# Kernel tuning notes

Hardware: AMD Instinct MI355X
Metric: run time of the kernel (lower is better)

The kernel has to match this reference:

```python
import jax, jax.numpy as jnp
import numpy as np

B, K, L, D, H = 128, 51, 60, 1, 32
NB = 2  # MAF blocks
LOG2PI = float(np.log(2.0 * np.pi))


def setup_inputs():
    kit = iter(jax.random.split(jax.random.key(0), 64))
    def nrm(shape, s=0.05):
        return jax.random.normal(next(kit), shape, dtype=jnp.float32) * s
    def uni(shape, lo, hi):
        return jax.random.uniform(next(kit), shape, dtype=jnp.float32, minval=lo, maxval=hi)
    c = L * D          # attention feature dim = 60
    KL = K * L         # 3060
    KL32 = KL * 32     # 97920
    return dict(
        x=jax.random.normal(next(kit), (B, K, L, D), dtype=jnp.float32),
        attn_Wq=nrm((c, c), 0.1), attn_bq=nrm((c,), 0.1),
        attn_Wk=nrm((c, c), 0.1), attn_bk=nrm((c,), 0.1),
        lstm_Wih=nrm((4 * H, D), 0.2), lstm_Whh=nrm((4 * H, H), 0.1),
        lstm_bih=nrm((4 * H,), 0.1), lstm_bhh=nrm((4 * H,), 0.1),
        gnn_Wn=nrm((H, H), 0.1), gnn_bn=nrm((H,), 0.1),
        gnn_Wr=nrm((H, H), 0.1),
        gnn_W2=nrm((H, H), 0.1), gnn_b2=nrm((H,), 0.1),
        mlp_W1=nrm((KL, 500), 0.02), mlp_b1=nrm((500,), 0.05),
        bn1_g=uni((500,), 0.8, 1.2), bn1_b=nrm((500,), 0.05),
        bn1_m=nrm((500,), 0.05), bn1_v=uni((500,), 0.5, 1.5),
        mlp_W2=nrm((500, 500), 0.05), mlp_b2=nrm((500,), 0.05),
        bn2_g=uni((500,), 0.8, 1.2), bn2_b=nrm((500,), 0.05),
        bn2_m=nrm((500,), 0.05), bn2_v=uni((500,), 0.5, 1.5),
        mlp_W3=nrm((500, KL32), 0.05), mlp_b3=nrm((KL32,), 0.05),
        ann_W=nrm((KL32, 100), 0.005), ann_b=nrm((100,), 0.05),
        annbn_g=uni((100,), 0.8, 1.2), annbn_b=nrm((100,), 0.05),
        annbn_m=nrm((100,), 0.05), annbn_v=uni((100,), 0.5, 1.5),
        maf_in_W=nrm((NB, H, D), 0.1), maf_in_b=nrm((NB, H), 0.1),
        maf_cond_W=nrm((NB, H, H), 0.1),
        maf_out_W=nrm((NB, 2 * D, H), 0.1), maf_out_b=nrm((NB, 2 * D), 0.1),
        maf_bn_lg=nrm((NB, D), 0.05), maf_bn_beta=nrm((NB, D), 0.05),
    )


def _forward(x, attn_Wq, attn_bq, attn_Wk, attn_bk,
             lstm_Wih, lstm_Whh, lstm_bih, lstm_bhh,
             gnn_Wn, gnn_bn, gnn_Wr, gnn_W2, gnn_b2,
             mlp_W1, mlp_b1, bn1_g, bn1_b, bn1_m, bn1_v,
             mlp_W2, mlp_b2, bn2_g, bn2_b, bn2_m, bn2_v,
             mlp_W3, mlp_b3,
             ann_W, ann_b, annbn_g, annbn_b, annbn_m, annbn_v,
             maf_in_W, maf_in_b, maf_cond_W, maf_out_W, maf_out_b,
             maf_bn_lg, maf_bn_beta):
    Bb, Kk, Ll, Dd = x.shape
    c = Ll * Dd
    # --- ScaleDotProductAttention (eval: dropout = identity) ---
    xf = x.reshape(Bb, Kk, c)
    q = xf @ attn_Wq + attn_bq
    k = xf @ attn_Wk + attn_bk
    k_t = k.reshape(Bb, c, Kk)                 # torch .view -- a reshape, NOT a transpose
    score = (q @ k_t) / jnp.sqrt(jnp.asarray(c, x.dtype))
    graph = jax.nn.softmax(score, axis=1)      # softmax over dim=1, (B,K,K)
    # --- single-layer LSTM over (B*K, L, D) ---
    xs = x.reshape(Bb * Kk, Ll, Dd)
    Hh = lstm_Whh.shape[1]
    def step(carry, xt):
        h, cc = carry
        z = xt @ lstm_Wih.T + lstm_bih + h @ lstm_Whh.T + lstm_bhh
        i, f, g, o = jnp.split(z, 4, axis=-1)  # torch gate order i,f,g,o
        cc = jax.nn.sigmoid(f) * cc + jax.nn.sigmoid(i) * jnp.tanh(g)
        h = jax.nn.sigmoid(o) * jnp.tanh(cc)
        return (h, cc), h
    h0 = jnp.zeros((Bb * Kk, Hh), dtype=x.dtype)
    _, hs = jax.lax.scan(step, (h0, h0), jnp.swapaxes(xs, 0, 1))
    h = jnp.swapaxes(hs, 0, 1).reshape(Bb, Kk, Ll, Hh)  # (B,K,L,H)
    # --- GNN message passing on attention-derived adjacency ---
    agg = jnp.einsum('bkld,bkj->bjld', h, graph)
    h_n = agg @ gnn_Wn + gnn_bn
    h_n = h_n.at[:, :, 1:].add(h[:, :, :-1] @ gnn_Wr)   # temporal shift residual
    h_gcn = jax.nn.relu(h_n) @ gnn_W2 + gnn_b2
    # --- gcn_mlp residual (BatchNorm1d in eval mode) ---
    bn = lambda z, g, b, m, v: (z - m) / jnp.sqrt(v + 1e-5) * g + b
    xflat = xs.reshape(Bb, -1)                          # (B, K*L*D)
    z = bn(jax.nn.relu(xflat @ mlp_W1 + mlp_b1), bn1_g, bn1_b, bn1_m, bn1_v)
    z = bn(jax.nn.relu(z @ mlp_W2 + mlp_b2), bn2_g, bn2_b, bn2_m, bn2_v)
    z = z @ mlp_W3 + mlp_b3
    h_gcn = z.reshape(h_gcn.shape) + h_gcn
    # --- ann head ---
    hid = bn(jax.nn.relu(h_gcn.reshape(Bb, -1) @ ann_W + ann_b),
             annbn_g, annbn_b, annbn_m, annbn_v)
    # --- conditional MAF log-prob over rows of (B*K*L, 1) with cond (., H) ---
    # input_size==1 => MADE output mask is all-zero (output degree -1 < hidden degree 0)
    u = xs.reshape(-1, Dd)
    cond = h_gcn.reshape(-1, h_gcn.shape[-1])
    mask_out = jnp.zeros((2 * Dd, Hh), dtype=x.dtype)
    sum_ldj = jnp.zeros_like(u)
    eps = 1e-5
    for i in range(maf_in_W.shape[0]):
        hm = jnp.tanh(u @ maf_in_W[i].T + maf_in_b[i] + cond @ maf_cond_W[i].T)
        out = hm @ (maf_out_W[i] * mask_out).T + maf_out_b[i]
        m, loga = out[:, :Dd], out[:, Dd:]
        u = (u - m) * jnp.exp(-loga)
        sum_ldj = sum_ldj - loga
        # flow BatchNorm, eval mode (running_mean=0, running_var=1 buffers)
        u = jnp.exp(maf_bn_lg[i]) * u * jax.lax.rsqrt(jnp.asarray(1.0 + eps, x.dtype)) + maf_bn_beta[i]
        sum_ldj = sum_ldj + maf_bn_lg[i] - 0.5 * jnp.log(jnp.asarray(1.0 + eps, x.dtype))
    logp_row = jnp.sum(-0.5 * LOG2PI - 0.5 * u * u + sum_ldj, axis=1)  # (B*K*L,)
    log_prob = logp_row.reshape(Bb, -1).mean(axis=1)    # (B,)
    return hid, log_prob, h_gcn


def reference(x, attn_Wq, attn_bq, attn_Wk, attn_bk,
              lstm_Wih, lstm_Whh, lstm_bih, lstm_bhh,
              gnn_Wn, gnn_bn, gnn_Wr, gnn_W2, gnn_b2,
              mlp_W1, mlp_b1, bn1_g, bn1_b, bn1_m, bn1_v,
              mlp_W2, mlp_b2, bn2_g, bn2_b, bn2_m, bn2_v,
              mlp_W3, mlp_b3,
              ann_W, ann_b, annbn_g, annbn_b, annbn_m, annbn_v,
              maf_in_W, maf_in_b, maf_cond_W, maf_out_W, maf_out_b,
              maf_bn_lg, maf_bn_beta):
    hid, log_prob, h_gcn = _forward(
        x, attn_Wq, attn_bq, attn_Wk, attn_bk,
        lstm_Wih, lstm_Whh, lstm_bih, lstm_bhh,
        gnn_Wn, gnn_bn, gnn_Wr, gnn_W2, gnn_b2,
        mlp_W1, mlp_b1, bn1_g, bn1_b, bn1_m, bn1_v,
        mlp_W2, mlp_b2, bn2_g, bn2_b, bn2_m, bn2_v,
        mlp_W3, mlp_b3,
        ann_W, ann_b, annbn_g, annbn_b, annbn_m, annbn_v,
        maf_in_W, maf_in_b, maf_cond_W, maf_out_W, maf_out_b,
        maf_bn_lg, maf_bn_beta)
    return (hid, log_prob.mean(), h_gcn, log_prob)
```

## Files before the change

kernel.cpp:

```cpp
#include <hip/hip_runtime.h>
#include <math.h>

constexpr int cB = 128;
constexpr int cK = 51;
constexpr int cL = 60;
constexpr int cH = 32;
constexpr int cC = 60;
constexpr int cKL = 3060;
constexpr int cKL32 = 97920;
constexpr float kLOG2PI = 1.8378770664093453f;

typedef __attribute__((ext_vector_type(8))) short bfrag8;
typedef __attribute__((ext_vector_type(16))) float accf16;
typedef __attribute__((ext_vector_type(4))) float accf4;
typedef __attribute__((ext_vector_type(4))) unsigned uint4v;

__device__ __forceinline__ float frcp(float x) { return __builtin_amdgcn_rcpf(x); }
__device__ __forceinline__ float fsig(float x) { return frcp(1.0f + __expf(-x)); }
__device__ __forceinline__ float ftanh(float x) {
  float e = __expf(2.0f * x);
  return 1.0f - 2.0f * frcp(e + 1.0f);
}
__device__ __forceinline__ short f2bf(float f) {
  union { float f; unsigned u; } v; v.f = f;
  unsigned r = v.u + 0x7FFFu + ((v.u >> 16) & 1u);
  return (short)(r >> 16);
}
__device__ __forceinline__ unsigned pk2bf(float lo, float hi) {
  unsigned r;
  asm("v_cvt_pk_bf16_f32 %0, %1, %2" : "=v"(r) : "v"(lo), "v"(hi));
  return r;
}

__global__ __launch_bounds__(256) void qk_kernel(
    const float* __restrict__ x, const float* __restrict__ Wq, const float* __restrict__ bq,
    const float* __restrict__ Wk, const float* __restrict__ bk,
    float* __restrict__ q, float* __restrict__ kx) {
  __shared__ float xs[8][cC];
  const int row0 = blockIdx.x * 8;
  const int tid = threadIdx.x;
  for (int idx = tid; idx < 8 * cC; idx += 256) {
    int lr = idx / cC, t = idx % cC;
    xs[lr][t] = x[(row0 + lr) * cC + t];
  }
  __syncthreads();
  for (int idx = tid; idx < 8 * 2 * cC; idx += 256) {
    int col = idx % cC;
    int r2 = idx / cC;
    int m = r2 & 1, lr = r2 >> 1;
    const float* W = m ? Wk : Wq;
    float acc = m ? bk[col] : bq[col];
    #pragma unroll 4
    for (int t = 0; t < cC; ++t) acc += xs[lr][t] * W[t * cC + col];
    float* outp = m ? kx : q;
    outp[(row0 + lr) * cC + col] = acc;
  }
}

__global__ __launch_bounds__(256) void attn_kernel(
    const float* __restrict__ q, const float* __restrict__ kx, float* __restrict__ graph) {
  __shared__ float qb[cKL];
  __shared__ float kb[cKL];
  __shared__ float sc[cK * cK];
  __shared__ float cmax[cK], csum[cK];
  const int b = blockIdx.x;
  const int tid = threadIdx.x;
  for (int idx = tid; idx < cKL; idx += 256) {
    qb[idx] = q[b * cKL + idx];
    kb[idx] = kx[b * cKL + idx];
  }
  __syncthreads();
  const float scale = 1.0f / sqrtf(60.0f);
  for (int idx = tid; idx < cK * cK; idx += 256) {
    int i = idx / cK, j = idx % cK;
    float acc = 0.0f;
    #pragma unroll 4
    for (int t = 0; t < cC; ++t) acc += qb[i * cC + t] * kb[t * cK + j];
    sc[idx] = acc * scale;
  }
  __syncthreads();
  if (tid < cK) {
    float m = -1e30f;
    for (int i = 0; i < cK; ++i) m = fmaxf(m, sc[i * cK + tid]);
    float ssum = 0.0f;
    for (int i = 0; i < cK; ++i) ssum += __expf(sc[i * cK + tid] - m);
    cmax[tid] = m; csum[tid] = ssum;
  }
  __syncthreads();
  for (int idx = tid; idx < cK * cK; idx += 256) {
    int j = idx % cK;
    graph[b * cK * cK + idx] = __expf(sc[idx] - cmax[j]) / csum[j];
  }
}

__global__ __launch_bounds__(64) void lstm_mfma_kernel(
    const float* __restrict__ x, const float* __restrict__ Wih, const float* __restrict__ Whh,
    const float* __restrict__ bih, const float* __restrict__ bhh, float* __restrict__ hout) {
  __shared__ float xlds[cL][16];
  __shared__ __align__(16) float hlds[16][36];
  const int lane = threadIdx.x;
  const int n = lane & 15;
  const int grp = lane >> 4;
  const int seq0 = blockIdx.x * 16;

  for (int i = lane; i < 16 * cL; i += 64) {
    const int s = i / cL, t = i % cL;
    xlds[t][s] = x[(size_t)(seq0 + s) * cL + t];
  }
  for (int i = lane; i < 16 * 36; i += 64) (&hlds[0][0])[i] = 0.0f;

  bfrag8 bf[8];
  float bias8[8], wih8[8];
  #pragma unroll
  for (int g = 0; g < 8; ++g) {
    const float* wrow = Whh + (g * 16 + n) * cH + grp * 8;
    const float4 p0 = *reinterpret_cast<const float4*>(wrow);
    const float4 p1 = *reinterpret_cast<const float4*>(wrow + 4);
    union { unsigned u[4]; bfrag8 b; } ub;
    ub.u[0] = pk2bf(p0.x, p0.y); ub.u[1] = pk2bf(p0.z, p0.w);
    ub.u[2] = pk2bf(p1.x, p1.y); ub.u[3] = pk2bf(p1.z, p1.w);
    bf[g] = ub.b;
    bias8[g] = bih[g * 16 + n] + bhh[g * 16 + n];
    wih8[g] = Wih[g * 16 + n];
  }
  float cst[8];
  #pragma unroll
  for (int i = 0; i < 8; ++i) cst[i] = 0.0f;
  __syncthreads();

  float* outp = hout + (size_t)seq0 * cL * cH;
  for (int t = 0; t < cL; ++t) {
    const float4 h0 = *reinterpret_cast<const float4*>(&hlds[n][grp * 8]);
    const float4 h1 = *reinterpret_cast<const float4*>(&hlds[n][grp * 8 + 4]);
    union { unsigned u[4]; bfrag8 b; } ua;
    ua.u[0] = pk2bf(h0.x, h0.y); ua.u[1] = pk2bf(h0.z, h0.w);
    ua.u[2] = pk2bf(h1.x, h1.y); ua.u[3] = pk2bf(h1.z, h1.w);
    const float4 xt = *reinterpret_cast<const float4*>(&xlds[t][grp * 4]);
    accf4 acc[8];
    #pragma unroll
    for (int g = 0; g < 8; ++g) {
      accf4 ci;
      ci[0] = fmaf(wih8[g], xt.x, bias8[g]);
      ci[1] = fmaf(wih8[g], xt.y, bias8[g]);
      ci[2] = fmaf(wih8[g], xt.z, bias8[g]);
      ci[3] = fmaf(wih8[g], xt.w, bias8[g]);
      acc[g] = __builtin_amdgcn_mfma_f32_16x16x32_bf16(ua.b, bf[g], ci, 0, 0, 0);
    }
    __builtin_amdgcn_sched_barrier(0);
    #pragma unroll
    for (int hh = 0; hh < 2; ++hh) {
      #pragma unroll
      for (int r = 0; r < 4; ++r) {
        const float iv = acc[0 + hh][r];
        const float fv = acc[2 + hh][r];
        const float gv = acc[4 + hh][r];
        const float ov = acc[6 + hh][r];
        float cs = cst[hh * 4 + r];
        cs = fmaf(fsig(fv), cs, fsig(iv) * ftanh(gv));
        const float hv = fsig(ov) * ftanh(cs);
        cst[hh * 4 + r] = cs;
        hlds[grp * 4 + r][n + hh * 16] = hv;
        outp[(size_t)(grp * 4 + r) * (cL * cH) + t * cH + n + hh * 16] = hv;
      }
    }
    __builtin_amdgcn_sched_barrier(0);
  }
}

__global__ __launch_bounds__(256) void agg_kernel(
    const float* __restrict__ hbuf, const float* __restrict__ graph,
    float* __restrict__ aggout) {
  __shared__ float G[cK * cK];
  __shared__ __align__(16) float Ht[cK][128];
  const int b = blockIdx.y;
  const int c0 = blockIdx.x * 128;
  const int tid = threadIdx.x;
  for (int idx = tid; idx < cK * cK; idx += 256) G[idx] = graph[b * cK * cK + idx];
  for (int idx = tid; idx < cK * 128; idx += 256) {
    int k = idx >> 7, c = idx & 127;
    Ht[k][c] = hbuf[((size_t)b * cK + k) * 1920 + c0 + c];
  }
  __syncthreads();
  const int jg = tid >> 5;
  const int cg = tid & 31;
  const int cc = cg * 4;
  float4 acc[7];
  #pragma unroll
  for (int jj = 0; jj < 7; ++jj) acc[jj] = make_float4(0.f, 0.f, 0.f, 0.f);
  for (int k = 0; k < cK; ++k) {
    const float4 hv = *reinterpret_cast<const float4*>(&Ht[k][cc]);
    #pragma unroll
    for (int jj = 0; jj < 7; ++jj) {
      const int j = jg + jj * 8;
      const float g = (j < cK) ? G[k * cK + j] : 0.0f;
      acc[jj].x += g * hv.x; acc[jj].y += g * hv.y;
      acc[jj].z += g * hv.z; acc[jj].w += g * hv.w;
    }
  }
  #pragma unroll
  for (int jj = 0; jj < 7; ++jj) {
    const int j = jg + jj * 8;
    if (j < cK) {
      const size_t o = ((size_t)b * cK + j) * 1920 + c0 + cc;
      aggout[o + 0] = acc[jj].x; aggout[o + 1] = acc[jj].y;
      aggout[o + 2] = acc[jj].z; aggout[o + 3] = acc[jj].w;
    }
  }
}

__global__ __launch_bounds__(256) void gnn2_kernel(
    const float* __restrict__ hbuf, const float* __restrict__ Wn,
    const float* __restrict__ bn_, const float* __restrict__ Wr,
    const float* __restrict__ W2, const float* __restrict__ b2,
    float* __restrict__ hg) {
  __shared__ __align__(16) float wn[cH * cH];
  __shared__ __align__(16) float wr[cH * cH];
  __shared__ __align__(16) float w2[cH * cH];
  __shared__ float bnb[cH], b2b[cH];
  __shared__ float A_[192][33];
  __shared__ float M_[192][33];
  const int tid = threadIdx.x;
  const int row0 = blockIdx.x * 192;
  for (int idx = tid; idx < cH * cH; idx += 256) { wn[idx] = Wn[idx]; wr[idx] = Wr[idx]; w2[idx] = W2[idx]; }
  if (tid < cH) { bnb[tid] = bn_[tid]; b2b[tid] = b2[tid]; }
  for (int idx = tid; idx < 192 * 32; idx += 256) {
    const int r = idx >> 5, d = idx & 31;
    A_[r][d] = hg[(size_t)(row0 + r) * 32 + d];
    const int g = row0 + r;
    const int l = g % 60;
    M_[r][d] = (l > 0) ? hbuf[(size_t)(g - 1) * 32 + d] : 0.0f;
  }
  __syncthreads();
  const int rg = tid >> 2;
  const int cg = tid & 3;
  const int c0 = cg * 8;
  const int r0 = rg * 3;
  float acc[3][8];
  #pragma unroll
  for (int i = 0; i < 3; ++i)
    #pragma unroll
    for (int d = 0; d < 8; ++d) acc[i][d] = bnb[c0 + d];
  for (int e = 0; e < cH; ++e) {
    const float4 wn0 = *reinterpret_cast<const float4*>(&wn[e * cH + c0]);
    const float4 wn1 = *reinterpret_cast<const float4*>(&wn[e * cH + c0 + 4]);
    const float4 wr0 = *reinterpret_cast<const float4*>(&wr[e * cH + c0]);
    const float4 wr1 = *reinterpret_cast<const float4*>(&wr[e * cH + c0 + 4]);
    #pragma unroll
    for (int i = 0; i < 3; ++i) {
      const float a = A_[r0 + i][e];
      const float m = M_[r0 + i][e];
      acc[i][0] += a * wn0.x + m * wr0.x; acc[i][1] += a * wn0.y + m * wr0.y;
      acc[i][2] += a * wn0.z + m * wr0.z; acc[i][3] += a * wn0.w + m * wr0.w;
      acc[i][4] += a * wn1.x + m * wr1.x; acc[i][5] += a * wn1.y + m * wr1.y;
      acc[i][6] += a * wn1.z + m * wr1.z; acc[i][7] += a * wn1.w + m * wr1.w;
    }
  }
  __syncthreads();
  #pragma unroll
  for (int i = 0; i < 3; ++i)
    #pragma unroll
    for (int d = 0; d < 8; ++d) A_[r0 + i][c0 + d] = fmaxf(acc[i][d], 0.0f);
  __syncthreads();
  float acc2[3][8];
  #pragma unroll
  for (int i = 0; i < 3; ++i)
    #pragma unroll
    for (int d = 0; d < 8; ++d) acc2[i][d] = b2b[c0 + d];
  for (int e = 0; e < cH; ++e) {
    const float4 w20 = *reinterpret_cast<const float4*>(&w2[e * cH + c0]);
    const float4 w21 = *reinterpret_cast<const float4*>(&w2[e * cH + c0 + 4]);
    #pragma unroll
    for (int i = 0; i < 3; ++i) {
      const float t = A_[r0 + i][e];
      acc2[i][0] += t * w20.x; acc2[i][1] += t * w20.y;
      acc2[i][2] += t * w20.z; acc2[i][3] += t * w20.w;
      acc2[i][4] += t * w21.x; acc2[i][5] += t * w21.y;
      acc2[i][6] += t * w21.z; acc2[i][7] += t * w21.w;
    }
  }
  #pragma unroll
  for (int i = 0; i < 3; ++i)
    #pragma unroll
    for (int d = 0; d < 8; ++d) M_[r0 + i][c0 + d] = acc2[i][d];
  __syncthreads();
  for (int idx = tid; idx < 192 * 32; idx += 256) {
    const int r = idx >> 5, d = idx & 31;
    hg[(size_t)row0 * 32 + idx] = M_[r][d];
  }
}

__global__ __launch_bounds__(256) void gemm_splitk_kernel(
    const float* __restrict__ A, const float* __restrict__ W,
    int K, int N, float* __restrict__ partial) {
  __shared__ __align__(16) float At[128][65];
  __shared__ __align__(16) float Wt[64][64];
  const int tid = threadIdx.x;
  const int n0 = blockIdx.x * 64;
  const int k0 = blockIdx.y * 64;
  const int kw = min(64, K - k0);
  for (int idx = tid; idx < 128 * 64; idx += 256) {
    int r = idx >> 6, kk = idx & 63;
    At[r][kk] = (kk < kw) ? A[(size_t)r * K + k0 + kk] : 0.0f;
  }
  for (int idx = tid; idx < 64 * 64; idx += 256) {
    int kk = idx >> 6, cc = idx & 63;
    Wt[kk][cc] = (kk < kw && n0 + cc < N) ? W[(size_t)(k0 + kk) * N + n0 + cc] : 0.0f;
  }
  __syncthreads();
  const int cg = tid & 15, rg = tid >> 4;
  const int c0 = cg * 4, r0 = rg * 8;
  float acc[8][4];
  #pragma unroll
  for (int i = 0; i < 8; ++i)
    #pragma unroll
    for (int jj = 0; jj < 4; ++jj) acc[i][jj] = 0.0f;
  for (int kk = 0; kk < 64; kk += 2) {
    const float4 wv0 = *reinterpret_cast<const float4*>(&Wt[kk][c0]);
    const float4 wv1 = *reinterpret_cast<const float4*>(&Wt[kk + 1][c0]);
    #pragma unroll
    for (int i = 0; i < 8; ++i) {
      const float2 av = *reinterpret_cast<const float2*>(&At[r0 + i][kk]);
      acc[i][0] += av.x * wv0.x + av.y * wv1.x;
      acc[i][1] += av.x * wv0.y + av.y * wv1.y;
      acc[i][2] += av.x * wv0.z + av.y * wv1.z;
      acc[i][3] += av.x * wv0.w + av.y * wv1.w;
    }
  }
  float* p = partial + (size_t)blockIdx.y * 128 * N;
  #pragma unroll
  for (int i = 0; i < 8; ++i) {
    #pragma unroll
    for (int jj = 0; jj < 4; ++jj) {
      const int cc = n0 + c0 + jj;
      if (cc < N) p[(r0 + i) * N + cc] = acc[i][jj];
    }
  }
}

__global__ __launch_bounds__(256) void mlpred_kernel(
    const float* __restrict__ partial, int S, int N,
    const float* __restrict__ bias, const float* __restrict__ gg,
    const float* __restrict__ bb, const float* __restrict__ mm,
    const float* __restrict__ vv, float* __restrict__ outz) {
  const int oi = blockIdx.x * 256 + threadIdx.x;
  if (oi >= 128 * N) return;
  float s = 0.0f;
  for (int p = 0; p < S; ++p) s += partial[(size_t)p * 128 * N + oi];
  const int c = oi % N;
  const float z = fmaxf(s + bias[c], 0.0f);
  outz[oi] = (z - mm[c]) * rsqrtf(vv[c] + 1e-5f) * gg[c] + bb[c];
}

__global__ __launch_bounds__(256) void mlpredbf_kernel(
    const float* __restrict__ partial, int S,
    const float* __restrict__ bias, const float* __restrict__ gg,
    const float* __restrict__ bb, const float* __restrict__ mm,
    const float* __restrict__ vv, unsigned short* __restrict__ outbf) {
  const int oi = blockIdx.x * 256 + threadIdx.x;
  if (oi >= 128 * 512) return;
  const int r = oi >> 9, c = oi & 511;
  unsigned short val = 0;
  if (c < 500) {
    float s = 0.0f;
    for (int p = 0; p < S; ++p) s += partial[(size_t)p * 64000 + r * 500 + c];
    const float z = fmaxf(s + bias[c], 0.0f);
    const float y = (z - mm[c]) * rsqrtf(vv[c] + 1e-5f) * gg[c] + bb[c];
    val = (unsigned short)f2bf(y);
  }
  outbf[oi] = val;
}

__global__ __launch_bounds__(256, 3) void w3_mfma_kernel(
    const unsigned short* __restrict__ z2bf, const float* __restrict__ W3,
    const float* __restrict__ b3, float* __restrict__ outh) {
  __shared__ unsigned Bs[2][16][128];
  const int tid = threadIdx.x;
  const int n0 = blockIdx.x * 128;
  const int wv = tid >> 6;
  const int lane = tid & 63;
  const int half = lane >> 5;
  const int lm = lane & 31;
  const int kp = tid >> 4;
  const int nc = (tid & 15) << 3;

  accf16 acc[4] = {};

  const unsigned short* Ab = z2bf + lm * 512 + half * 8;
  const float* Wp = W3 + (size_t)(2 * kp) * cKL32 + n0 + nc;

  {
    const float4 r0a = *reinterpret_cast<const float4*>(Wp);
    const float4 r0b = *reinterpret_cast<const float4*>(Wp + 4);
    const float4 r1a = *reinterpret_cast<const float4*>(Wp + cKL32);
    const float4 r1b = *reinterpret_cast<const float4*>(Wp + cKL32 + 4);
    uint4v w0 = {pk2bf(r0a.x, r1a.x), pk2bf(r0a.y, r1a.y), pk2bf(r0a.z, r1a.z), pk2bf(r0a.w, r1a.w)};
    uint4v w1 = {pk2bf(r0b.x, r1b.x), pk2bf(r0b.y, r1b.y), pk2bf(r0b.z, r1b.z), pk2bf(r0b.w, r1b.w)};
    *reinterpret_cast<uint4v*>(&Bs[0][kp][nc]) = w0;
    *reinterpret_cast<uint4v*>(&Bs[0][kp][nc + 4]) = w1;
  }
  __syncthreads();

  int cur = 0;
  for (int t = 0; t < 16; ++t) {
    const int k0 = t << 5;
    bfrag8 a0[4], a1[4];
    #pragma unroll
    for (int mf = 0; mf < 4; ++mf) {
      a0[mf] = *reinterpret_cast<const bfrag8*>(Ab + mf * 16384 + k0);
      a1[mf] = *reinterpret_cast<const bfrag8*>(Ab + mf * 16384 + k0 + 16);
    }
    float4 r0a = make_float4(0.f, 0.f, 0.f, 0.f), r0b = r0a, r1a = r0a, r1b = r0a;
    if (t < 15) {
      const int kA = k0 + 32 + 2 * kp;
      const float* p = Wp + (size_t)(k0 + 32) * cKL32;
      if (kA < 500)     { r0a = *reinterpret_cast<const float4*>(p);
                          r0b = *reinterpret_cast<const float4*>(p + 4); }
      if (kA + 1 < 500) { r1a = *reinterpret_cast<const float4*>(p + cKL32);
                          r1b = *reinterpret_cast<const float4*>(p + cKL32 + 4); }
    }
    const unsigned* Bf = &Bs[cur][0][0];
    const int colL = wv * 32 + lm;
    union { unsigned u[4]; bfrag8 b; } cv0, cv1;
    #pragma unroll
    for (int c = 0; c < 4; ++c) cv0.u[c] = Bf[(half * 4 + c) * 128 + colL];
    #pragma unroll
    for (int c = 0; c < 4; ++c) cv1.u[c] = Bf[(8 + half * 4 + c) * 128 + colL];
    #pragma unroll
    for (int mf = 0; mf < 4; ++mf)
      acc[mf] = __builtin_amdgcn_mfma_f32_32x32x16_bf16(a0[mf], cv0.b, acc[mf], 0, 0, 0);
    #pragma unroll
    for (int mf = 0; mf < 4; ++mf)
      acc[mf] = __builtin_amdgcn_mfma_f32_32x32x16_bf16(a1[mf], cv1.b, acc[mf], 0, 0, 0);
    if (t < 15) {
      uint4v w0 = {pk2bf(r0a.x, r1a.x), pk2bf(r0a.y, r1a.y), pk2bf(r0a.z, r1a.z), pk2bf(r0a.w, r1a.w)};
      uint4v w1 = {pk2bf(r0b.x, r1b.x), pk2bf(r0b.y, r1b.y), pk2bf(r0b.z, r1b.z), pk2bf(r0b.w, r1b.w)};
      *reinterpret_cast<uint4v*>(&Bs[cur ^ 1][kp][nc]) = w0;
      *reinterpret_cast<uint4v*>(&Bs[cur ^ 1][kp][nc + 4]) = w1;
    }
    __syncthreads();
    cur ^= 1;
  }

  const int col = n0 + wv * 32 + lm;
  const float bias = b3[col];
  #pragma unroll
  for (int mf = 0; mf < 4; ++mf) {
    #pragma unroll
    for (int reg = 0; reg < 16; ++reg) {
      const int rr = mf * 32 + (reg & 3) + 8 * (reg >> 2) + 4 * half;
      const size_t o = (size_t)rr * cKL32 + col;
      outh[o] += acc[mf][reg] + bias;
    }
  }
}

__global__ __launch_bounds__(256, 3) void ann_mfma_kernel(
    const float* __restrict__ hg, const float* __restrict__ annW,
    float* __restrict__ partial) {
  __shared__ unsigned Bs[2][16][128];
  const int tid = threadIdx.x;
  const int bx = blockIdx.x;
  const int kbase = bx * 128;
  const int wv = tid >> 6;
  const int lane = tid & 63;
  const int half = lane >> 5;
  const int lm = lane & 31;

  accf16 acc[4] = {};

  #pragma unroll
  for (int i = 0; i < 8; ++i) {
    const int idx = tid + i * 256;
    const int kp = idx >> 7, col = idx & 127;
    float w0 = 0.f, w1 = 0.f;
    if (col < 100) {
      const size_t base = (size_t)(kbase + 2 * kp) * 100 + col;
      w0 = annW[base];
      w1 = annW[base + 100];
    }
    Bs[0][kp][col] = pk2bf(w0, w1);
  }
  __syncthreads();

  const float* Ap = hg + (size_t)lm * cKL32 + kbase + half * 8;
  int cur = 0;
  for (int t = 0; t < 4; ++t) {
    const int k0 = t * 32;
    bfrag8 a0[4], a1[4];
    #pragma unroll
    for (int mf = 0; mf < 4; ++mf) {
      const float* p = Ap + (size_t)mf * 32 * cKL32 + k0;
      const float4 f0 = *reinterpret_cast<const float4*>(p);
      const float4 f1 = *reinterpret_cast<const float4*>(p + 4);
      const float4 g0 = *reinterpret_cast<const float4*>(p + 16);
      const float4 g1 = *reinterpret_cast<const float4*>(p + 20);
      union { unsigned u[4]; bfrag8 b; } ua, ub;
      ua.u[0] = pk2bf(f0.x, f0.y); ua.u[1] = pk2bf(f0.z, f0.w);
      ua.u[2] = pk2bf(f1.x, f1.y); ua.u[3] = pk2bf(f1.z, f1.w);
      ub.u[0] = pk2bf(g0.x, g0.y); ub.u[1] = pk2bf(g0.z, g0.w);
      ub.u[2] = pk2bf(g1.x, g1.y); ub.u[3] = pk2bf(g1.z, g1.w);
      a0[mf] = ua.b; a1[mf] = ub.b;
    }
    float w0r[8], w1r[8];
    if (t < 3) {
      #pragma unroll
      for (int i = 0; i < 8; ++i) {
        const int idx = tid + i * 256;
        const int kp = idx >> 7, col = idx & 127;
        w0r[i] = 0.f; w1r[i] = 0.f;
        if (col < 100) {
          const size_t base = (size_t)(kbase + (t + 1) * 32 + 2 * kp) * 100 + col;
          w0r[i] = annW[base];
          w1r[i] = annW[base + 100];
        }
      }
    }
    const unsigned* Bf = &Bs[cur][0][0];
    const int colL = wv * 32 + lm;
    union { unsigned u[4]; bfrag8 b; } cv0, cv1;
    #pragma unroll
    for (int c = 0; c < 4; ++c) cv0.u[c] = Bf[(half * 4 + c) * 128 + colL];
    #pragma unroll
    for (int c = 0; c < 4; ++c) cv1.u[c] = Bf[(8 + half * 4 + c) * 128 + colL];
    #pragma unroll
    for (int mf = 0; mf < 4; ++mf)
      acc[mf] = __builtin_amdgcn_mfma_f32_32x32x16_bf16(a0[mf], cv0.b, acc[mf], 0, 0, 0);
    #pragma unroll
    for (int mf = 0; mf < 4; ++mf)
      acc[mf] = __builtin_amdgcn_mfma_f32_32x32x16_bf16(a1[mf], cv1.b, acc[mf], 0, 0, 0);
    if (t < 3) {
      #pragma unroll
      for (int i = 0; i < 8; ++i) {
        const int idx = tid + i * 256;
        const int kp = idx >> 7, col = idx & 127;
        Bs[cur ^ 1][kp][col] = pk2bf(w0r[i], w1r[i]);
      }
    }
    __syncthreads();
    cur ^= 1;
  }

  const int col = wv * 32 + lm;
  if (col < 100) {
    float* p = partial + (size_t)bx * 12800;
    #pragma unroll
    for (int mf = 0; mf < 4; ++mf) {
      #pragma unroll
      for (int reg = 0; reg < 16; ++reg) {
        const int rr = mf * 32 + (reg & 3) + 8 * (reg >> 2) + 4 * half;
        p[rr * 100 + col] = acc[mf][reg];
      }
    }
  }
}

__global__ __launch_bounds__(256) void annred1_kernel(
    const float* __restrict__ partial, float* __restrict__ partial2) {
  const int oi = blockIdx.x * 256 + threadIdx.x;
  const int by = blockIdx.y;
  if (oi >= 12800) return;
  const float* p = partial + (size_t)(by * 51) * 12800 + oi;
  float s = 0.0f;
  #pragma unroll 4
  for (int q = 0; q < 51; ++q) s += p[(size_t)q * 12800];
  partial2[(size_t)by * 12800 + oi] = s;
}

__global__ __launch_bounds__(256) void annred2_kernel(
    const float* __restrict__ partial2, const float* __restrict__ ab,
    const float* __restrict__ gg, const float* __restrict__ bb,
    const float* __restrict__ mm, const float* __restrict__ vv, float* __restrict__ hid) {
  const int oi = blockIdx.x * 256 + threadIdx.x;
  if (oi < 12800) {
    float s = 0.0f;
    #pragma unroll
    for (int p = 0; p < 15; ++p) s += partial2[(size_t)p * 12800 + oi];
    const int c = oi % 100;
    const float z = fmaxf(s + ab[c], 0.0f);
    hid[oi] = (z - mm[c]) * rsqrtf(vv[c] + 1e-5f) * gg[c] + bb[c];
  }
}

__global__ __launch_bounds__(256) void logp_kernel(
    const float* __restrict__ x, const float* __restrict__ mob,
    const float* __restrict__ mlg, const float* __restrict__ mbeta, float* __restrict__ lp) {
  const int b = blockIdx.x;
  const int tid = threadIdx.x;
  const float rs = rsqrtf(1.0f + 1e-5f);
  const float A0 = __expf(mlg[0] - mob[1]) * rs;
  const float B0 = -mob[0] * __expf(-mob[1]) * __expf(mlg[0]) * rs + mbeta[0];
  const float A1 = __expf(mlg[1] - mob[3]) * rs;
  const float B1 = -mob[2] * __expf(-mob[3]) * __expf(mlg[1]) * rs + mbeta[1];
  const float S = (mlg[0] - mob[1]) + (mlg[1] - mob[3]) - logf(1.0f + 1e-5f);
  const float a = A1 * A0;
  const float bc = A1 * B0 + B1;
  float s = 0.0f;
  for (int t = tid; t < cKL; t += 256) {
    const float u = a * x[b * cKL + t] + bc;
    s += u * u;
  }
  #pragma unroll
  for (int off = 32; off > 0; off >>= 1) s += __shfl_down(s, off);
  __shared__ float red[4];
  if ((tid & 63) == 0) red[tid >> 6] = s;
  __syncthreads();
  if (tid == 0) {
    const float tot = red[0] + red[1] + red[2] + red[3];
    lp[b] = -0.5f * tot / (float)cKL + (-0.5f * kLOG2PI + S);
  }
}

__global__ void lpmean_kernel(const float* __restrict__ lp, float* __restrict__ outm) {
  __shared__ float red[128];
  const int tid = threadIdx.x;
  red[tid] = lp[tid];
  __syncthreads();
  for (int off = 64; off > 0; off >>= 1) {
    if (tid < off) red[tid] += red[tid + off];
    __syncthreads();
  }
  if (tid == 0) outm[0] = red[0] / 128.0f;
}

extern "C" void kernel_launch(void* const* d_in, const int* in_sizes, int n_in,
                              void* d_out, int out_size, void* d_ws, size_t ws_size,
                              hipStream_t stream) {
  const float* x    = (const float*)d_in[0];
  const float* Wq   = (const float*)d_in[1];
  const float* bq   = (const float*)d_in[2];
  const float* Wk   = (const float*)d_in[3];
  const float* bk   = (const float*)d_in[4];
  const float* Wih  = (const float*)d_in[5];
  const float* Whh  = (const float*)d_in[6];
  const float* bih  = (const float*)d_in[7];
  const float* bhh  = (const float*)d_in[8];
  const float* gWn  = (const float*)d_in[9];
  const float* gbn  = (const float*)d_in[10];
  const float* gWr  = (const float*)d_in[11];
  const float* gW2  = (const float*)d_in[12];
  const float* gb2  = (const float*)d_in[13];
  const float* W1   = (const float*)d_in[14];
  const float* b1   = (const float*)d_in[15];
  const float* bn1g = (const float*)d_in[16];
  const float* bn1b = (const float*)d_in[17];
  const float* bn1m = (const float*)d_in[18];
  const float* bn1v = (const float*)d_in[19];
  const float* W2m  = (const float*)d_in[20];
  const float* b2m  = (const float*)d_in[21];
  const float* bn2g = (const float*)d_in[22];
  const float* bn2b = (const float*)d_in[23];
  const float* bn2m = (const float*)d_in[24];
  const float* bn2v = (const float*)d_in[25];
  const float* W3   = (const float*)d_in[26];
  const float* b3   = (const float*)d_in[27];
  const float* annW = (const float*)d_in[28];
  const float* annb = (const float*)d_in[29];
  const float* abg  = (const float*)d_in[30];
  const float* abb  = (const float*)d_in[31];
  const float* abm  = (const float*)d_in[32];
  const float* abv  = (const float*)d_in[33];
  const float* mob  = (const float*)d_in[38];
  const float* mlg  = (const float*)d_in[39];
  const float* mbeta= (const float*)d_in[40];

  float* ws = (float*)d_ws;
  float* qb    = ws;
  float* kb    = ws + 391680;
  float* graph = ws + 783360;
  float* hbuf  = ws + 1116288;
  float* z1    = ws + 13650048;
  unsigned short* z2bf = (unsigned short*)(ws + 13714048);
  float* partial  = hbuf;
  float* partial2 = hbuf + 10000000;
  float* mp    = hbuf + 4000000;

  float* outF = (float*)d_out;
  float* hid  = outF;
  float* lpm  = outF + 12800;
  float* hgcn = outF + 12801;
  float* lp   = outF + 12546561;

  qk_kernel<<<816, 256, 0, stream>>>(x, Wq, bq, Wk, bk, qb, kb);
  attn_kernel<<<128, 256, 0, stream>>>(qb, kb, graph);
  lstm_mfma_kernel<<<408, 64, 0, stream>>>(x, Wih, Whh, bih, bhh, hbuf);
  agg_kernel<<<dim3(15, 128), 256, 0, stream>>>(hbuf, graph, hgcn);
  gnn2_kernel<<<2040, 256, 0, stream>>>(hbuf, gWn, gbn, gWr, gW2, gb2, hgcn);
  gemm_splitk_kernel<<<dim3(8, 48), 256, 0, stream>>>(x, W1, 3060, 500, mp);
  mlpred_kernel<<<250, 256, 0, stream>>>(mp, 48, 500, b1, bn1g, bn1b, bn1m, bn1v, z1);
  gemm_splitk_kernel<<<dim3(8, 8), 256, 0, stream>>>(z1, W2m, 500, 500, mp);
  mlpredbf_kernel<<<256, 256, 0, stream>>>(mp, 8, b2m, bn2g, bn2b, bn2m, bn2v, z2bf);
  w3_mfma_kernel<<<765, 256, 0, stream>>>(z2bf, W3, b3, hgcn);
  ann_mfma_kernel<<<765, 256, 0, stream>>>(hgcn, annW, partial);
  annred1_kernel<<<dim3(50, 15), 256, 0, stream>>>(partial, partial2);
  annred2_kernel<<<50, 256, 0, stream>>>(partial2, annb, abg, abb, abm, abv, hid);
  logp_kernel<<<128, 256, 0, stream>>>(x, mob, mlg, mbeta, lp);
  lpmean_kernel<<<1, 128, 0, stream>>>(lp, lpm);
}
```

Measured before the change: 747.7 us.

## Fuse QK projection into attention kernel and deepen ann split-K to drop a reduction

The Q/K projection is folded into the attention kernel, so each batch block computes q and k in shared memory and the intermediate global buffers and one launch go away. The ann split-K GEMM now covers 384 K-elements per block (255 blocks instead of 765), which shrinks the partial buffer so a single reduction kernel replaces the two-stage reduction. The trade-off is lower parallelism: QK work now runs on only 128 blocks, the ann GEMM has fewer blocks, and the final reduction is a longer serial loop over 255 partials.

Result: slower. 781.8 us (+4.6%).

```diff
diff --git a/kernel.cpp b/kernel.cpp
--- a/kernel.cpp
+++ b/kernel.cpp
@@ -32,42 +32,37 @@
   return r;
 }
 
-__global__ __launch_bounds__(256) void qk_kernel(
+__global__ __launch_bounds__(256) void qkattn_kernel(
     const float* __restrict__ x, const float* __restrict__ Wq, const float* __restrict__ bq,
-    const float* __restrict__ Wk, const float* __restrict__ bk,
-    float* __restrict__ q, float* __restrict__ kx) {
-  __shared__ float xs[8][cC];
-  const int row0 = blockIdx.x * 8;
-  const int tid = threadIdx.x;
-  for (int idx = tid; idx < 8 * cC; idx += 256) {
-    int lr = idx / cC, t = idx % cC;
-    xs[lr][t] = x[(row0 + lr) * cC + t];
-  }
-  __syncthreads();
-  for (int idx = tid; idx < 8 * 2 * cC; idx += 256) {
-    int col = idx % cC;
-    int r2 = idx / cC;
-    int m = r2 & 1, lr = r2 >> 1;
-    const float* W = m ? Wk : Wq;
-    float acc = m ? bk[col] : bq[col];
-    #pragma unroll 4
-    for (int t = 0; t < cC; ++t) acc += xs[lr][t] * W[t * cC + col];
-    float* outp = m ? kx : q;
-    outp[(row0 + lr) * cC + col] = acc;
-  }
-}
-
-__global__ __launch_bounds__(256) void attn_kernel(
-    const float* __restrict__ q, const float* __restrict__ kx, float* __restrict__ graph) {
-  __shared__ float qb[cKL];
+    const float* __restrict__ Wk, const float* __restrict__ bk, float* __restrict__ graph) {
+  __shared__ float xs[cK][cC];
+  __shared__ float Wl[cC * cC];
+  __shared__ float qs[cK][cC];
   __shared__ float kb[cKL];
   __shared__ float sc[cK * cK];
   __shared__ float cmax[cK], csum[cK];
   const int b = blockIdx.x;
   const int tid = threadIdx.x;
-  for (int idx = tid; idx < cKL; idx += 256) {
-    qb[idx] = q[b * cKL + idx];
-    kb[idx] = kx[b * cKL + idx];
+  for (int idx = tid; idx < cK * cC; idx += 256)
+    xs[idx / cC][idx % cC] = x[(size_t)b * cKL + idx];
+  for (int idx = tid; idx < cC * cC; idx += 256) Wl[idx] = Wq[idx];
+  __syncthreads();
+  for (int idx = tid; idx < cK * cC; idx += 256) {
+    const int i = idx / cC, col = idx % cC;
+    float acc = bq[col];
+    #pragma unroll 4
+    for (int t = 0; t < cC; ++t) acc += xs[i][t] * Wl[t * cC + col];
+    qs[i][col] = acc;
+  }
+  __syncthreads();
+  for (int idx = tid; idx < cC * cC; idx += 256) Wl[idx] = Wk[idx];
+  __syncthreads();
+  for (int idx = tid; idx < cK * cC; idx += 256) {
+    const int i = idx / cC, col = idx % cC;
+    float acc = bk[col];
+    #pragma unroll 4
+    for (int t = 0; t < cC; ++t) acc += xs[i][t] * Wl[t * cC + col];
+    kb[idx] = acc;
   }
   __syncthreads();
   const float scale = 1.0f / sqrtf(60.0f);
@@ -75,7 +70,7 @@
     int i = idx / cK, j = idx % cK;
     float acc = 0.0f;
     #pragma unroll 4
-    for (int t = 0; t < cC; ++t) acc += qb[i * cC + t] * kb[t * cK + j];
+    for (int t = 0; t < cC; ++t) acc += qs[i][t] * kb[t * cK + j];
     sc[idx] = acc * scale;
   }
   __syncthreads();
@@ -460,7 +455,7 @@
   __shared__ unsigned Bs[2][16][128];
   const int tid = threadIdx.x;
   const int bx = blockIdx.x;
-  const int kbase = bx * 128;
+  const int kbase = bx * 384;
   const int wv = tid >> 6;
   const int lane = tid & 63;
   const int half = lane >> 5;
@@ -484,7 +479,7 @@
 
   const float* Ap = hg + (size_t)lm * cKL32 + kbase + half * 8;
   int cur = 0;
-  for (int t = 0; t < 4; ++t) {
+  for (int t = 0; t < 12; ++t) {
     const int k0 = t * 32;
     bfrag8 a0[4], a1[4];
     #pragma unroll
@@ -502,7 +497,7 @@
       a0[mf] = ua.b; a1[mf] = ub.b;
     }
     float w0r[8], w1r[8];
-    if (t < 3) {
+    if (t < 11) {
       #pragma unroll
       for (int i = 0; i < 8; ++i) {
         const int idx = tid + i * 256;
@@ -528,7 +523,7 @@
     #pragma unroll
     for (int mf = 0; mf < 4; ++mf)
       acc[mf] = __builtin_amdgcn_mfma_f32_32x32x16_bf16(a1[mf], cv1.b, acc[mf], 0, 0, 0);
-    if (t < 3) {
+    if (t < 11) {
       #pragma unroll
       for (int i = 0; i < 8; ++i) {
         const int idx = tid + i * 256;
@@ -554,27 +549,15 @@
   }
 }
 
-__global__ __launch_bounds__(256) void annred1_kernel(
-    const float* __restrict__ partial, float* __restrict__ partial2) {
-  const int oi = blockIdx.x * 256 + threadIdx.x;
-  const int by = blockIdx.y;
-  if (oi >= 12800) return;
-  const float* p = partial + (size_t)(by * 51) * 12800 + oi;
-  float s = 0.0f;
-  #pragma unroll 4
-  for (int q = 0; q < 51; ++q) s += p[(size_t)q * 12800];
-  partial2[(size_t)by * 12800 + oi] = s;
-}
-
-__global__ __launch_bounds__(256) void annred2_kernel(
-    const float* __restrict__ partial2, const float* __restrict__ ab,
+__global__ __launch_bounds__(256) void annred_kernel(
+    const float* __restrict__ partial, const float* __restrict__ ab,
     const float* __restrict__ gg, const float* __restrict__ bb,
     const float* __restrict__ mm, const float* __restrict__ vv, float* __restrict__ hid) {
   const int oi = blockIdx.x * 256 + threadIdx.x;
   if (oi < 12800) {
     float s = 0.0f;
-    #pragma unroll
-    for (int p = 0; p < 15; ++p) s += partial2[(size_t)p * 12800 + oi];
+    #pragma unroll 5
+    for (int p = 0; p < 255; ++p) s += partial[(size_t)p * 12800 + oi];
     const int c = oi % 100;
     const float z = fmaxf(s + ab[c], 0.0f);
     hid[oi] = (z - mm[c]) * rsqrtf(vv[c] + 1e-5f) * gg[c] + bb[c];
@@ -664,14 +647,11 @@
   const float* mbeta= (const float*)d_in[40];
 
   float* ws = (float*)d_ws;
-  float* qb    = ws;
-  float* kb    = ws + 391680;
   float* graph = ws + 783360;
   float* hbuf  = ws + 1116288;
   float* z1    = ws + 13650048;
   unsigned short* z2bf = (unsigned short*)(ws + 13714048);
   float* partial  = hbuf;
-  float* partial2 = hbuf + 10000000;
   float* mp    = hbuf + 4000000;
 
   float* outF = (float*)d_out;
@@ -680,8 +660,7 @@
   float* hgcn = outF + 12801;
   float* lp   = outF + 12546561;
 
-  qk_kernel<<<816, 256, 0, stream>>>(x, Wq, bq, Wk, bk, qb, kb);
-  attn_kernel<<<128, 256, 0, stream>>>(qb, kb, graph);
+  qkattn_kernel<<<128, 256, 0, stream>>>(x, Wq, bq, Wk, bk, graph);
   lstm_mfma_kernel<<<408, 64, 0, stream>>>(x, Wih, Whh, bih, bhh, hbuf);
   agg_kernel<<<dim3(15, 128), 256, 0, stream>>>(hbuf, graph, hgcn);
   gnn2_kernel<<<2040, 256, 0, stream>>>(hbuf, gWn, gbn, gWr, gW2, gb2, hgcn);
@@ -690,9 +669,8 @@
   gemm_splitk_kernel<<<dim3(8, 8), 256, 0, stream>>>(z1, W2m, 500, 500, mp);
   mlpredbf_kernel<<<256, 256, 0, stream>>>(mp, 8, b2m, bn2g, bn2b, bn2m, bn2v, z2bf);
   w3_mfma_kernel<<<765, 256, 0, stream>>>(z2bf, W3, b3, hgcn);
-  ann_mfma_kernel<<<765, 256, 0, stream>>>(hgcn, annW, partial);
-  annred1_kernel<<<dim3(50, 15), 256, 0, stream>>>(partial, partial2);
-  annred2_kernel<<<50, 256, 0, stream>>>(partial2, annb, abg, abb, abm, abv, hid);
+  ann_mfma_kernel<<<255, 256, 0, stream>>>(hgcn, annW, partial);
+  annred_kernel<<<50, 256, 0, stream>>>(partial, annb, abg, abb, abm, abv, hid);
   logp_kernel<<<128, 256, 0, stream>>>(x, mob, mlg, mbeta, lp);
   lpmean_kernel<<<1, 128, 0, stream>>>(lp, lpm);
 }
```
